# Kernel optimization log

Measured on AMD Instinct MI355X. Metric: run time of the kernel, lower is better.

Reference implementation:

```python
import jax, jax.numpy as jnp
import numpy as np


def setup_inputs() -> dict:
    key = jax.random.key(0)
    k1, k2, k3, k4 = jax.random.split(key, 4)
    d_in, d_out, r = 4096, 4096, 16
    n_tok = 8192  # batch 4 * seq 2048
    x = jax.random.normal(k1, (n_tok, d_in), dtype=jnp.float32)
    W = jax.random.normal(k2, (d_out, d_in), dtype=jnp.float32)
    A = jax.random.normal(k3, (d_out, r), dtype=jnp.float32)
    B = jax.random.normal(k4, (r, d_in), dtype=jnp.float32)
    return {"x": x, "W": W, "A": A, "B": B}


def reference(x, W, A, B):
    # Faithful to torch: F.linear(x, W + A @ B) = x @ (W + A @ B)^T, no bias.
    W_eff = W + A @ B  # [d_out, d_in], materialized as in the original module
    return x @ W_eff.T  # [n_tok, d_out]
```

## Files before the change

### kernel.cpp

```cpp
#include <hip/hip_runtime.h>

typedef __attribute__((ext_vector_type(8))) short short8;
typedef __attribute__((ext_vector_type(4))) float f32x4;
typedef unsigned short ushort_t;

#define BAR()   __builtin_amdgcn_s_barrier()
#define LGKM0() asm volatile("s_waitcnt lgkmcnt(0)" ::: "memory")
#define VM6()   asm volatile("s_waitcnt vmcnt(6)" ::: "memory")
#define VM0()   asm volatile("s_waitcnt vmcnt(0)" ::: "memory")
#define PRIO(n) __builtin_amdgcn_s_setprio(n)
#define MFMA(a_, b_, c_) __builtin_amdgcn_mfma_f32_16x16x32_bf16(a_, b_, c_, 0, 0, 0)

__device__ __forceinline__ unsigned short f2bf(float f) {
  unsigned u = __builtin_bit_cast(unsigned, f);
  u += 0x7FFFu + ((u >> 16) & 1u);
  return (unsigned short)(u >> 16);
}

__device__ __forceinline__ void gl_lds16(const void* g, void* l) {
  __builtin_amdgcn_global_load_lds(
      (const __attribute__((address_space(1))) void*)g,
      (__attribute__((address_space(3))) void*)l, 16, 0, 0);
}

__global__ __launch_bounds__(256) void cvt_x(const float* __restrict__ x,
                                             ushort_t* __restrict__ xb) {
  size_t i = ((size_t)blockIdx.x * 256 + threadIdx.x) * 8;
  float4 v0 = *(const float4*)(x + i);
  float4 v1 = *(const float4*)(x + i + 4);
  union { ushort_t s[8]; uint4 v; } o;
  o.s[0] = f2bf(v0.x); o.s[1] = f2bf(v0.y); o.s[2] = f2bf(v0.z); o.s[3] = f2bf(v0.w);
  o.s[4] = f2bf(v1.x); o.s[5] = f2bf(v1.y); o.s[6] = f2bf(v1.z); o.s[7] = f2bf(v1.w);
  *(uint4*)(xb + i) = o.v;
}

__global__ __launch_bounds__(256) void build_weff(const float* __restrict__ W,
                                                  const float* __restrict__ A,
                                                  const float* __restrict__ B,
                                                  ushort_t* __restrict__ Weff) {
  const int K = 4096, R = 16;
  const int n = blockIdx.y;
  const int k = (blockIdx.x * 256 + threadIdx.x) * 4;
  float4 w = *(const float4*)(W + (size_t)n * K + k);
  float a0 = w.x, a1 = w.y, a2 = w.z, a3 = w.w;
#pragma unroll
  for (int r = 0; r < R; ++r) {
    float a = A[n * R + r];
    float4 b = *(const float4*)(B + (size_t)r * K + k);
    a0 += a * b.x; a1 += a * b.y; a2 += a * b.z; a3 += a * b.w;
  }
  union { ushort_t s[4]; uint2 v; } o;
  o.s[0] = f2bf(a0); o.s[1] = f2bf(a1); o.s[2] = f2bf(a2); o.s[3] = f2bf(a3);
  *(uint2*)(Weff + (size_t)n * K + k) = o.v;
}


__device__ __forceinline__ void stage_half(const ushort_t* __restrict__ G, int row0, int kc,
                                           ushort_t* half, int tid) {
#pragma unroll
  for (int r = 0; r < 2; ++r) {
    const int idx  = r * 512 + tid;
    const int lrow = idx >> 2;
    const int cb   = ((idx & 3) * 16) ^ (((lrow >> 3) & 1) << 5);
    const ushort_t* src = G + (size_t)(row0 + lrow) * 4096 + kc + (cb >> 1);
    char* dst = (char*)half + (size_t)(r * 512 + (tid & ~63)) * 16;
    gl_lds16(src, dst);
  }
}

__global__ __launch_bounds__(512, 2) void gemm256(const ushort_t* __restrict__ Xb,
                                                  const ushort_t* __restrict__ Wb,
                                                  float* __restrict__ C) {
  const int N = 4096;
  const int NT = 4096 / 64;
  __shared__ __align__(16) ushort_t lds[2][4][256 * 32];

  const int tid = threadIdx.x;
  const int l   = tid & 63;
  const int w   = tid >> 6;
  const int wm  = w >> 2;
  const int wn  = w & 3;

  const int bid = blockIdx.x;
  const int c = bid & 7, q = bid >> 3;
  const int tm = (c >> 1) * 8 + (q >> 3);
  const int tn = (c & 1) * 8 + (q & 7);
  const int bm = tm * 256, bn = tn * 256;

  const int colb = ((l >> 4) * 16) ^ (((l >> 3) & 1) << 5);
  int aoff[8], boff[4];
#pragma unroll
  for (int mi = 0; mi < 8; ++mi) aoff[mi] = (wm * 128 + mi * 16 + (l & 15)) * 64 + colb;
#pragma unroll
  for (int ni = 0; ni < 4; ++ni) boff[ni] = (wn * 64 + ni * 16 + (l & 15)) * 64 + colb;

  f32x4 acc[8][4];
#pragma unroll
  for (int i = 0; i < 8; ++i)
#pragma unroll
    for (int j = 0; j < 4; ++j) acc[i][j] = (f32x4)(0.0f);

  stage_half(Wb, bn, 0,  lds[0][2], tid);
  stage_half(Xb, bm, 0,  lds[0][0], tid);
  stage_half(Wb, bn, 32, lds[0][3], tid);
  stage_half(Xb, bm, 32, lds[0][1], tid);
  stage_half(Wb, bn, 64, lds[1][2], tid);
  stage_half(Xb, bm, 64, lds[1][0], tid);
  stage_half(Wb, bn, 96, lds[1][3], tid);
  VM6();
  BAR();

  short8 af0, af1, af2, af3, bf0, bf1, bf2, bf3;

#define LDA(P_, I0_) do { \
    af0 = *(const short8*)((const char*)(P_) + aoff[(I0_) + 0]); \
    af1 = *(const short8*)((const char*)(P_) + aoff[(I0_) + 1]); \
    af2 = *(const short8*)((const char*)(P_) + aoff[(I0_) + 2]); \
    af3 = *(const short8*)((const char*)(P_) + aoff[(I0_) + 3]); \
  } while (0)
#define LDB(P_) do { \
    bf0 = *(const short8*)((const char*)(P_) + boff[0]); \
    bf1 = *(const short8*)((const char*)(P_) + boff[1]); \
    bf2 = *(const short8*)((const char*)(P_) + boff[2]); \
    bf3 = *(const short8*)((const char*)(P_) + boff[3]); \
  } while (0)
#define QUAD(M0_) do { \
    acc[(M0_)+0][0] = MFMA(af0, bf0, acc[(M0_)+0][0]); \
    acc[(M0_)+0][1] = MFMA(af0, bf1, acc[(M0_)+0][1]); \
    acc[(M0_)+0][2] = MFMA(af0, bf2, acc[(M0_)+0][2]); \
    acc[(M0_)+0][3] = MFMA(af0, bf3, acc[(M0_)+0][3]); \
    acc[(M0_)+1][0] = MFMA(af1, bf0, acc[(M0_)+1][0]); \
    acc[(M0_)+1][1] = MFMA(af1, bf1, acc[(M0_)+1][1]); \
    acc[(M0_)+1][2] = MFMA(af1, bf2, acc[(M0_)+1][2]); \
    acc[(M0_)+1][3] = MFMA(af1, bf3, acc[(M0_)+1][3]); \
    acc[(M0_)+2][0] = MFMA(af2, bf0, acc[(M0_)+2][0]); \
    acc[(M0_)+2][1] = MFMA(af2, bf1, acc[(M0_)+2][1]); \
    acc[(M0_)+2][2] = MFMA(af2, bf2, acc[(M0_)+2][2]); \
    acc[(M0_)+2][3] = MFMA(af2, bf3, acc[(M0_)+2][3]); \
    acc[(M0_)+3][0] = MFMA(af3, bf0, acc[(M0_)+3][0]); \
    acc[(M0_)+3][1] = MFMA(af3, bf1, acc[(M0_)+3][1]); \
    acc[(M0_)+3][2] = MFMA(af3, bf2, acc[(M0_)+3][2]); \
    acc[(M0_)+3][3] = MFMA(af3, bf3, acc[(M0_)+3][3]); \
  } while (0)

  int cur = 0;
  for (int t = 0; t < NT; ++t) {
    const ushort_t* A0h = lds[cur][0];
    const ushort_t* A1h = lds[cur][1];
    const ushort_t* B0h = lds[cur][2];
    const ushort_t* B1h = lds[cur][3];
    const int kc2 = (t + 2) * 64;

    LDA(A0h, 0); LDB(B0h);
    if (t + 1 < NT) stage_half(Xb, bm, (t + 1) * 64 + 32, lds[cur ^ 1][1], tid);
    BAR(); LGKM0(); PRIO(1);
    QUAD(0);
    PRIO(0); BAR();

    LDA(A0h, 4);
    if (t + 2 < NT) stage_half(Wb, bn, kc2, lds[cur][2], tid);
    BAR(); LGKM0(); PRIO(1);
    QUAD(4);
    PRIO(0); BAR();

    LDA(A1h, 0); LDB(B1h);
    if (t + 2 < NT) stage_half(Xb, bm, kc2, lds[cur][0], tid);
    BAR(); LGKM0(); PRIO(1);
    QUAD(0);
    PRIO(0); BAR();

    LDA(A1h, 4);
    if (t + 2 < NT) stage_half(Wb, bn, kc2 + 32, lds[cur][3], tid);
    if (t + 2 < NT) { VM6(); } else { VM0(); }
    BAR(); LGKM0(); PRIO(1);
    QUAD(4);
    PRIO(0); BAR();

    cur ^= 1;
  }

  const int erow = bm + wm * 128 + (l >> 4) * 4;
  const int ecol = bn + wn * 64 + (l & 15);
#pragma unroll
  for (int mi = 0; mi < 8; ++mi) {
#pragma unroll
    for (int ni = 0; ni < 4; ++ni) {
      float* cp = C + (size_t)(erow + mi * 16) * N + ecol + ni * 16;
#pragma unroll
      for (int j = 0; j < 4; ++j) cp[(size_t)j * N] = acc[mi][ni][j];
    }
  }
}

extern "C" void kernel_launch(void* const* d_in, const int* in_sizes, int n_in,
                              void* d_out, int out_size, void* d_ws, size_t ws_size,
                              hipStream_t stream) {
  const float* x = (const float*)d_in[0];
  const float* W = (const float*)d_in[1];
  const float* A = (const float*)d_in[2];
  const float* B = (const float*)d_in[3];
  float* out = (float*)d_out;

  ushort_t* xb = (ushort_t*)d_ws;
  ushort_t* wb = (ushort_t*)((char*)d_ws + (size_t)8192 * 4096 * 2);

  cvt_x<<<16384, 256, 0, stream>>>(x, xb);
  dim3 gw(4, 4096);
  build_weff<<<gw, 256, 0, stream>>>(W, A, B, wb);
  gemm256<<<512, 512, 0, stream>>>(xb, wb, out);
}
```

Baseline: 333.7 us.

## Restructure GEMM main loop to single-barrier double buffer with register-level fragment prefetch

Replaces the two-stage-ahead, four-barrier-per-step ping-pong schedule with a simpler loop: the whole next k-tile is staged into the alternate LDS buffer at the start of each step, and a single vmcnt(0)+barrier sits at the end. LDS fragment reads are double-buffered in registers and interleaved with MFMA groups using sched_barrier fences. The intent is to cut barrier overhead and let LDS reads overlap MFMAs, at the cost of shallower global prefetch depth and higher register use. The launch bound's minimum-blocks hint is dropped.

```diff
diff --git a/kernel.cpp b/kernel.cpp
--- a/kernel.cpp
+++ b/kernel.cpp
@@ -5,9 +5,8 @@
 typedef unsigned short ushort_t;
 
 #define BAR()   __builtin_amdgcn_s_barrier()
-#define LGKM0() asm volatile("s_waitcnt lgkmcnt(0)" ::: "memory")
-#define VM6()   asm volatile("s_waitcnt vmcnt(6)" ::: "memory")
 #define VM0()   asm volatile("s_waitcnt vmcnt(0)" ::: "memory")
+#define SB()    __builtin_amdgcn_sched_barrier(0)
 #define PRIO(n) __builtin_amdgcn_s_setprio(n)
 #define MFMA(a_, b_, c_) __builtin_amdgcn_mfma_f32_16x16x32_bf16(a_, b_, c_, 0, 0, 0)
 
@@ -68,9 +67,9 @@
   }
 }
 
-__global__ __launch_bounds__(512, 2) void gemm256(const ushort_t* __restrict__ Xb,
-                                                  const ushort_t* __restrict__ Wb,
-                                                  float* __restrict__ C) {
+__global__ __launch_bounds__(512) void gemm256(const ushort_t* __restrict__ Xb,
+                                               const ushort_t* __restrict__ Wb,
+                                               float* __restrict__ C) {
   const int N = 4096;
   const int NT = 4096 / 64;
   __shared__ __align__(16) ushort_t lds[2][4][256 * 32];
@@ -104,43 +103,49 @@
   stage_half(Xb, bm, 0,  lds[0][0], tid);
   stage_half(Wb, bn, 32, lds[0][3], tid);
   stage_half(Xb, bm, 32, lds[0][1], tid);
-  stage_half(Wb, bn, 64, lds[1][2], tid);
-  stage_half(Xb, bm, 64, lds[1][0], tid);
-  stage_half(Wb, bn, 96, lds[1][3], tid);
-  VM6();
+  VM0();
   BAR();
 
-  short8 af0, af1, af2, af3, bf0, bf1, bf2, bf3;
-
-#define LDA(P_, I0_) do { \
-    af0 = *(const short8*)((const char*)(P_) + aoff[(I0_) + 0]); \
-    af1 = *(const short8*)((const char*)(P_) + aoff[(I0_) + 1]); \
-    af2 = *(const short8*)((const char*)(P_) + aoff[(I0_) + 2]); \
-    af3 = *(const short8*)((const char*)(P_) + aoff[(I0_) + 3]); \
-  } while (0)
-#define LDB(P_) do { \
-    bf0 = *(const short8*)((const char*)(P_) + boff[0]); \
-    bf1 = *(const short8*)((const char*)(P_) + boff[1]); \
-    bf2 = *(const short8*)((const char*)(P_) + boff[2]); \
-    bf3 = *(const short8*)((const char*)(P_) + boff[3]); \
-  } while (0)
-#define QUAD(M0_) do { \
-    acc[(M0_)+0][0] = MFMA(af0, bf0, acc[(M0_)+0][0]); \
-    acc[(M0_)+0][1] = MFMA(af0, bf1, acc[(M0_)+0][1]); \
-    acc[(M0_)+0][2] = MFMA(af0, bf2, acc[(M0_)+0][2]); \
-    acc[(M0_)+0][3] = MFMA(af0, bf3, acc[(M0_)+0][3]); \
-    acc[(M0_)+1][0] = MFMA(af1, bf0, acc[(M0_)+1][0]); \
-    acc[(M0_)+1][1] = MFMA(af1, bf1, acc[(M0_)+1][1]); \
-    acc[(M0_)+1][2] = MFMA(af1, bf2, acc[(M0_)+1][2]); \
-    acc[(M0_)+1][3] = MFMA(af1, bf3, acc[(M0_)+1][3]); \
-    acc[(M0_)+2][0] = MFMA(af2, bf0, acc[(M0_)+2][0]); \
-    acc[(M0_)+2][1] = MFMA(af2, bf1, acc[(M0_)+2][1]); \
-    acc[(M0_)+2][2] = MFMA(af2, bf2, acc[(M0_)+2][2]); \
-    acc[(M0_)+2][3] = MFMA(af2, bf3, acc[(M0_)+2][3]); \
-    acc[(M0_)+3][0] = MFMA(af3, bf0, acc[(M0_)+3][0]); \
-    acc[(M0_)+3][1] = MFMA(af3, bf1, acc[(M0_)+3][1]); \
-    acc[(M0_)+3][2] = MFMA(af3, bf2, acc[(M0_)+3][2]); \
-    acc[(M0_)+3][3] = MFMA(af3, bf3, acc[(M0_)+3][3]); \
+  short8 a1_0, a1_1, a1_2, a1_3;
+  short8 a2_0, a2_1, a2_2, a2_3;
+  short8 b1_0, b1_1, b1_2, b1_3;
+  short8 b2_0, b2_1, b2_2, b2_3;
+
+#define RD_A1(P_) do { \
+    a1_0 = *(const short8*)((const char*)(P_) + aoff[0]); \
+    a1_1 = *(const short8*)((const char*)(P_) + aoff[1]); \
+    a1_2 = *(const short8*)((const char*)(P_) + aoff[2]); \
+    a1_3 = *(const short8*)((const char*)(P_) + aoff[3]); \
+  } while (0)
+#define RD_A2(P_) do { \
+    a2_0 = *(const short8*)((const char*)(P_) + aoff[4]); \
+    a2_1 = *(const short8*)((const char*)(P_) + aoff[5]); \
+    a2_2 = *(const short8*)((const char*)(P_) + aoff[6]); \
+    a2_3 = *(const short8*)((const char*)(P_) + aoff[7]); \
+  } while (0)
+#define RD_B(P_, B0_, B1_, B2_, B3_) do { \
+    B0_ = *(const short8*)((const char*)(P_) + boff[0]); \
+    B1_ = *(const short8*)((const char*)(P_) + boff[1]); \
+    B2_ = *(const short8*)((const char*)(P_) + boff[2]); \
+    B3_ = *(const short8*)((const char*)(P_) + boff[3]); \
+  } while (0)
+#define QUAD(M0_, A0_, A1_, A2_, A3_, B0_, B1_, B2_, B3_) do { \
+    acc[(M0_)+0][0] = MFMA(A0_, B0_, acc[(M0_)+0][0]); \
+    acc[(M0_)+0][1] = MFMA(A0_, B1_, acc[(M0_)+0][1]); \
+    acc[(M0_)+0][2] = MFMA(A0_, B2_, acc[(M0_)+0][2]); \
+    acc[(M0_)+0][3] = MFMA(A0_, B3_, acc[(M0_)+0][3]); \
+    acc[(M0_)+1][0] = MFMA(A1_, B0_, acc[(M0_)+1][0]); \
+    acc[(M0_)+1][1] = MFMA(A1_, B1_, acc[(M0_)+1][1]); \
+    acc[(M0_)+1][2] = MFMA(A1_, B2_, acc[(M0_)+1][2]); \
+    acc[(M0_)+1][3] = MFMA(A1_, B3_, acc[(M0_)+1][3]); \
+    acc[(M0_)+2][0] = MFMA(A2_, B0_, acc[(M0_)+2][0]); \
+    acc[(M0_)+2][1] = MFMA(A2_, B1_, acc[(M0_)+2][1]); \
+    acc[(M0_)+2][2] = MFMA(A2_, B2_, acc[(M0_)+2][2]); \
+    acc[(M0_)+2][3] = MFMA(A2_, B3_, acc[(M0_)+2][3]); \
+    acc[(M0_)+3][0] = MFMA(A3_, B0_, acc[(M0_)+3][0]); \
+    acc[(M0_)+3][1] = MFMA(A3_, B1_, acc[(M0_)+3][1]); \
+    acc[(M0_)+3][2] = MFMA(A3_, B2_, acc[(M0_)+3][2]); \
+    acc[(M0_)+3][3] = MFMA(A3_, B3_, acc[(M0_)+3][3]); \
   } while (0)
 
   int cur = 0;
@@ -149,33 +154,34 @@
     const ushort_t* A1h = lds[cur][1];
     const ushort_t* B0h = lds[cur][2];
     const ushort_t* B1h = lds[cur][3];
-    const int kc2 = (t + 2) * 64;
-
-    LDA(A0h, 0); LDB(B0h);
-    if (t + 1 < NT) stage_half(Xb, bm, (t + 1) * 64 + 32, lds[cur ^ 1][1], tid);
-    BAR(); LGKM0(); PRIO(1);
-    QUAD(0);
-    PRIO(0); BAR();
-
-    LDA(A0h, 4);
-    if (t + 2 < NT) stage_half(Wb, bn, kc2, lds[cur][2], tid);
-    BAR(); LGKM0(); PRIO(1);
-    QUAD(4);
-    PRIO(0); BAR();
-
-    LDA(A1h, 0); LDB(B1h);
-    if (t + 2 < NT) stage_half(Xb, bm, kc2, lds[cur][0], tid);
-    BAR(); LGKM0(); PRIO(1);
-    QUAD(0);
-    PRIO(0); BAR();
-
-    LDA(A1h, 4);
-    if (t + 2 < NT) stage_half(Wb, bn, kc2 + 32, lds[cur][3], tid);
-    if (t + 2 < NT) { VM6(); } else { VM0(); }
-    BAR(); LGKM0(); PRIO(1);
-    QUAD(4);
-    PRIO(0); BAR();
-
+
+    if (t + 1 < NT) {
+      const int kc = (t + 1) * 64;
+      stage_half(Wb, bn, kc,      lds[cur ^ 1][2], tid);
+      stage_half(Xb, bm, kc,      lds[cur ^ 1][0], tid);
+      stage_half(Wb, bn, kc + 32, lds[cur ^ 1][3], tid);
+      stage_half(Xb, bm, kc + 32, lds[cur ^ 1][1], tid);
+    }
+
+    RD_A1(A0h);
+    RD_B(B0h, b1_0, b1_1, b1_2, b1_3);
+    RD_A2(A0h);
+    SB();
+    PRIO(1); QUAD(0, a1_0, a1_1, a1_2, a1_3, b1_0, b1_1, b1_2, b1_3); PRIO(0);
+    SB();
+    RD_A1(A1h);
+    RD_B(B1h, b2_0, b2_1, b2_2, b2_3);
+    SB();
+    PRIO(1); QUAD(4, a2_0, a2_1, a2_2, a2_3, b1_0, b1_1, b1_2, b1_3); PRIO(0);
+    SB();
+    RD_A2(A1h);
+    SB();
+    PRIO(1); QUAD(0, a1_0, a1_1, a1_2, a1_3, b2_0, b2_1, b2_2, b2_3); PRIO(0);
+    SB();
+    PRIO(1); QUAD(4, a2_0, a2_1, a2_2, a2_3, b2_0, b2_1, b2_2, b2_3); PRIO(0);
+    SB();
+    VM0();
+    BAR();
     cur ^= 1;
   }
 
```

New measurement: 333.6 us. About the same (-0.0%).

## Restage GEMM tiles as row-halves with full-K rows and register-reused fragments

Applied to the files above, without the earlier changes.

Changes the LDS staging so each half-buffer holds 128 rows by the full 64-wide K slice, not 256 rows by 32 K, with a new XOR swizzle. Each wave now loads A fragments for both K halves and reuses them across two B column passes, cutting LDS reads per MFMA. The stage schedule is reordered so both W halves are issued together in the last phase. The occupancy hint of 2 blocks per CU is removed from launch bounds, which frees register pressure but may lower occupancy.

```diff
diff --git a/kernel.cpp b/kernel.cpp
--- a/kernel.cpp
+++ b/kernel.cpp
@@ -6,6 +6,7 @@
 
 #define BAR()   __builtin_amdgcn_s_barrier()
 #define LGKM0() asm volatile("s_waitcnt lgkmcnt(0)" ::: "memory")
+#define LGKM8() asm volatile("s_waitcnt lgkmcnt(8)" ::: "memory")
 #define VM6()   asm volatile("s_waitcnt vmcnt(6)" ::: "memory")
 #define VM0()   asm volatile("s_waitcnt vmcnt(0)" ::: "memory")
 #define PRIO(n) __builtin_amdgcn_s_setprio(n)
@@ -55,25 +56,26 @@
 }
 
 
-__device__ __forceinline__ void stage_half(const ushort_t* __restrict__ G, int row0, int kc,
+__device__ __forceinline__ void stage_half(const ushort_t* __restrict__ G, int grow0, int kc,
                                            ushort_t* half, int tid) {
 #pragma unroll
   for (int r = 0; r < 2; ++r) {
-    const int idx  = r * 512 + tid;
-    const int lrow = idx >> 2;
-    const int cb   = ((idx & 3) * 16) ^ (((lrow >> 3) & 1) << 5);
-    const ushort_t* src = G + (size_t)(row0 + lrow) * 4096 + kc + (cb >> 1);
-    char* dst = (char*)half + (size_t)(r * 512 + (tid & ~63)) * 16;
+    const int P = (r * 512 + tid) * 16;
+    const int L = P ^ (((P >> 9) & 1) << 5);
+    const int row = L >> 7;
+    const int colb = L & 127;
+    const ushort_t* src = G + (size_t)(grow0 + row) * 4096 + kc + (colb >> 1);
+    char* dst = (char*)half + (size_t)((r * 512 + (tid & ~63)) * 16);
     gl_lds16(src, dst);
   }
 }
 
-__global__ __launch_bounds__(512, 2) void gemm256(const ushort_t* __restrict__ Xb,
-                                                  const ushort_t* __restrict__ Wb,
-                                                  float* __restrict__ C) {
+__global__ __launch_bounds__(512) void gemm256(const ushort_t* __restrict__ Xb,
+                                               const ushort_t* __restrict__ Wb,
+                                               float* __restrict__ C) {
   const int N = 4096;
   const int NT = 4096 / 64;
-  __shared__ __align__(16) ushort_t lds[2][4][256 * 32];
+  __shared__ __align__(16) ushort_t lds[2][4][128 * 64];
 
   const int tid = threadIdx.x;
   const int l   = tid & 63;
@@ -87,12 +89,7 @@
   const int tn = (c & 1) * 8 + (q & 7);
   const int bm = tm * 256, bn = tn * 256;
 
-  const int colb = ((l >> 4) * 16) ^ (((l >> 3) & 1) << 5);
-  int aoff[8], boff[4];
-#pragma unroll
-  for (int mi = 0; mi < 8; ++mi) aoff[mi] = (wm * 128 + mi * 16 + (l & 15)) * 64 + colb;
-#pragma unroll
-  for (int ni = 0; ni < 4; ++ni) boff[ni] = (wn * 64 + ni * 16 + (l & 15)) * 64 + colb;
+  const int rb = (((l & 15) * 128) + ((l >> 4) * 16)) ^ (((l >> 2) & 1) << 5);
 
   f32x4 acc[8][4];
 #pragma unroll
@@ -100,80 +97,95 @@
 #pragma unroll
     for (int j = 0; j < 4; ++j) acc[i][j] = (f32x4)(0.0f);
 
-  stage_half(Wb, bn, 0,  lds[0][2], tid);
-  stage_half(Xb, bm, 0,  lds[0][0], tid);
-  stage_half(Wb, bn, 32, lds[0][3], tid);
-  stage_half(Xb, bm, 32, lds[0][1], tid);
-  stage_half(Wb, bn, 64, lds[1][2], tid);
-  stage_half(Xb, bm, 64, lds[1][0], tid);
-  stage_half(Wb, bn, 96, lds[1][3], tid);
+  stage_half(Wb, bn,       0,  lds[0][2], tid);
+  stage_half(Xb, bm,       0,  lds[0][0], tid);
+  stage_half(Wb, bn + 128, 0,  lds[0][3], tid);
+  stage_half(Xb, bm + 128, 0,  lds[0][1], tid);
+  stage_half(Wb, bn,       64, lds[1][2], tid);
+  stage_half(Xb, bm,       64, lds[1][0], tid);
+  stage_half(Wb, bn + 128, 64, lds[1][3], tid);
   VM6();
   BAR();
 
-  short8 af0, af1, af2, af3, bf0, bf1, bf2, bf3;
-
-#define LDA(P_, I0_) do { \
-    af0 = *(const short8*)((const char*)(P_) + aoff[(I0_) + 0]); \
-    af1 = *(const short8*)((const char*)(P_) + aoff[(I0_) + 1]); \
-    af2 = *(const short8*)((const char*)(P_) + aoff[(I0_) + 2]); \
-    af3 = *(const short8*)((const char*)(P_) + aoff[(I0_) + 3]); \
-  } while (0)
-#define LDB(P_) do { \
-    bf0 = *(const short8*)((const char*)(P_) + boff[0]); \
-    bf1 = *(const short8*)((const char*)(P_) + boff[1]); \
-    bf2 = *(const short8*)((const char*)(P_) + boff[2]); \
-    bf3 = *(const short8*)((const char*)(P_) + boff[3]); \
-  } while (0)
-#define QUAD(M0_) do { \
-    acc[(M0_)+0][0] = MFMA(af0, bf0, acc[(M0_)+0][0]); \
-    acc[(M0_)+0][1] = MFMA(af0, bf1, acc[(M0_)+0][1]); \
-    acc[(M0_)+0][2] = MFMA(af0, bf2, acc[(M0_)+0][2]); \
-    acc[(M0_)+0][3] = MFMA(af0, bf3, acc[(M0_)+0][3]); \
-    acc[(M0_)+1][0] = MFMA(af1, bf0, acc[(M0_)+1][0]); \
-    acc[(M0_)+1][1] = MFMA(af1, bf1, acc[(M0_)+1][1]); \
-    acc[(M0_)+1][2] = MFMA(af1, bf2, acc[(M0_)+1][2]); \
-    acc[(M0_)+1][3] = MFMA(af1, bf3, acc[(M0_)+1][3]); \
-    acc[(M0_)+2][0] = MFMA(af2, bf0, acc[(M0_)+2][0]); \
-    acc[(M0_)+2][1] = MFMA(af2, bf1, acc[(M0_)+2][1]); \
-    acc[(M0_)+2][2] = MFMA(af2, bf2, acc[(M0_)+2][2]); \
-    acc[(M0_)+2][3] = MFMA(af2, bf3, acc[(M0_)+2][3]); \
-    acc[(M0_)+3][0] = MFMA(af3, bf0, acc[(M0_)+3][0]); \
-    acc[(M0_)+3][1] = MFMA(af3, bf1, acc[(M0_)+3][1]); \
-    acc[(M0_)+3][2] = MFMA(af3, bf2, acc[(M0_)+3][2]); \
-    acc[(M0_)+3][3] = MFMA(af3, bf3, acc[(M0_)+3][3]); \
-  } while (0)
+  short8 a[8][2];
+  short8 bb[2][2];
+
+#define RD(P_) (*(const short8*)(P_))
 
   int cur = 0;
   for (int t = 0; t < NT; ++t) {
-    const ushort_t* A0h = lds[cur][0];
-    const ushort_t* A1h = lds[cur][1];
-    const ushort_t* B0h = lds[cur][2];
-    const ushort_t* B1h = lds[cur][3];
-    const int kc2 = (t + 2) * 64;
-
-    LDA(A0h, 0); LDB(B0h);
-    if (t + 1 < NT) stage_half(Xb, bm, (t + 1) * 64 + 32, lds[cur ^ 1][1], tid);
+    const char* Ab = (const char*)lds[cur][wm] + rb;
+    const char* Bb = (const char*)lds[cur][2 + (wn >> 1)] + (wn & 1) * 8192 + rb;
+    const int kc1 = (t + 1) * 64, kc2 = (t + 2) * 64;
+
+#pragma unroll
+    for (int mi = 0; mi < 4; ++mi) {
+      a[mi][0] = RD(Ab + mi * 2048);
+      a[mi][1] = RD(Ab + mi * 2048 + 64);
+    }
+#pragma unroll
+    for (int ni = 0; ni < 2; ++ni) {
+      bb[ni][0] = RD(Bb + ni * 2048);
+      bb[ni][1] = RD(Bb + ni * 2048 + 64);
+    }
+    if (t + 1 < NT) stage_half(Xb, bm + 128, kc1, lds[cur ^ 1][1], tid);
+    LGKM8();
     BAR(); LGKM0(); PRIO(1);
-    QUAD(0);
-    PRIO(0); BAR();
-
-    LDA(A0h, 4);
-    if (t + 2 < NT) stage_half(Wb, bn, kc2, lds[cur][2], tid);
+#pragma unroll
+    for (int kh = 0; kh < 2; ++kh)
+#pragma unroll
+      for (int mi = 0; mi < 4; ++mi)
+#pragma unroll
+        for (int ni = 0; ni < 2; ++ni)
+          acc[mi][ni] = MFMA(a[mi][kh], bb[ni][kh], acc[mi][ni]);
+    PRIO(0); BAR();
+
+#pragma unroll
+    for (int mi = 4; mi < 8; ++mi) {
+      a[mi][0] = RD(Ab + mi * 2048);
+      a[mi][1] = RD(Ab + mi * 2048 + 64);
+    }
     BAR(); LGKM0(); PRIO(1);
-    QUAD(4);
-    PRIO(0); BAR();
-
-    LDA(A1h, 0); LDB(B1h);
+#pragma unroll
+    for (int kh = 0; kh < 2; ++kh)
+#pragma unroll
+      for (int mi = 4; mi < 8; ++mi)
+#pragma unroll
+        for (int ni = 0; ni < 2; ++ni)
+          acc[mi][ni] = MFMA(a[mi][kh], bb[ni][kh], acc[mi][ni]);
+    PRIO(0); BAR();
+
+#pragma unroll
+    for (int ni = 0; ni < 2; ++ni) {
+      bb[ni][0] = RD(Bb + (2 + ni) * 2048);
+      bb[ni][1] = RD(Bb + (2 + ni) * 2048 + 64);
+    }
     if (t + 2 < NT) stage_half(Xb, bm, kc2, lds[cur][0], tid);
     BAR(); LGKM0(); PRIO(1);
-    QUAD(0);
-    PRIO(0); BAR();
-
-    LDA(A1h, 4);
-    if (t + 2 < NT) stage_half(Wb, bn, kc2 + 32, lds[cur][3], tid);
-    if (t + 2 < NT) { VM6(); } else { VM0(); }
-    BAR(); LGKM0(); PRIO(1);
-    QUAD(4);
+#pragma unroll
+    for (int kh = 0; kh < 2; ++kh)
+#pragma unroll
+      for (int mi = 0; mi < 4; ++mi)
+#pragma unroll
+        for (int ni = 0; ni < 2; ++ni)
+          acc[mi][ni + 2] = MFMA(a[mi][kh], bb[ni][kh], acc[mi][ni + 2]);
+    PRIO(0); BAR();
+
+    if (t + 2 < NT) {
+      stage_half(Wb, bn,       kc2, lds[cur][2], tid);
+      stage_half(Wb, bn + 128, kc2, lds[cur][3], tid);
+      VM6();
+    } else {
+      VM0();
+    }
+    BAR(); PRIO(1);
+#pragma unroll
+    for (int kh = 0; kh < 2; ++kh)
+#pragma unroll
+      for (int mi = 4; mi < 8; ++mi)
+#pragma unroll
+        for (int ni = 0; ni < 2; ++ni)
+          acc[mi][ni + 2] = MFMA(a[mi][kh], bb[ni][kh], acc[mi][ni + 2]);
     PRIO(0); BAR();
 
     cur ^= 1;
```

Result: slower. 344.8 us (+3.3%).
